# Optimization experiments

Hardware: AMD Instinct MI355X
Metric: run time of the kernel (lower is better)

The kernel has to match this reference:

```python
import jax, jax.numpy as jnp
import numpy as np

D_MODEL = 192
DEPTH = 16
D_INNER = 384   # expand=2
D_STATE = 16
D_CONV = 4
DT_RANK = 12    # ceil(192/16)
J = 42
T = 8
NUM_CLASSES = 1000
B = 64
EPS = 1e-5


def setup_inputs() -> dict:
    key = jax.random.key(0)
    ks = jax.random.split(key, 16)

    def n(k, shape, scale=0.02):
        return jax.random.normal(k, shape, jnp.float32) * scale

    dt_bias_init = float(np.log(np.expm1(0.01)))  # softplus^-1(0.01), mamba dt init
    A_init = jnp.log(jnp.tile(jnp.arange(1, D_STATE + 1, dtype=jnp.float32), (DEPTH, D_INNER, 1)))
    return {
        "x": jax.random.normal(ks[0], (B, T, J, 3), jnp.float32),
        "joint_embed_w": n(ks[1], (D_MODEL, 3)),
        "joint_embed_b": jnp.zeros((D_MODEL,), jnp.float32),
        "cls_token": n(ks[2], (1, 1, D_MODEL)),
        "spatial_pos": n(ks[3], (1, J + 1, D_MODEL)),
        "temporal_pos": n(ks[4], (1, T, D_MODEL)),
        "norm_w": jnp.ones((DEPTH, D_MODEL), jnp.float32),
        "in_proj_w": n(ks[5], (DEPTH, 2 * D_INNER, D_MODEL)),
        "conv_w": n(ks[6], (DEPTH, D_INNER, D_CONV), 0.1),
        "conv_b": jnp.zeros((DEPTH, D_INNER), jnp.float32),
        "x_proj_w": n(ks[7], (DEPTH, DT_RANK + 2 * D_STATE, D_INNER)),
        "dt_proj_w": n(ks[8], (DEPTH, D_INNER, DT_RANK), DT_RANK ** -0.5),
        "dt_proj_b": jnp.full((DEPTH, D_INNER), dt_bias_init, jnp.float32),
        "A_log": A_init,
        "Dp": jnp.ones((DEPTH, D_INNER), jnp.float32),
        "out_proj_w": n(ks[9], (DEPTH, D_MODEL, D_INNER)),
        "norm_f_w": jnp.ones((D_MODEL,), jnp.float32),
        "head_w": n(ks[10], (NUM_CLASSES, D_MODEL)),
        "head_b": jnp.zeros((NUM_CLASSES,), jnp.float32),
    }


def rmsnorm(x, w):
    return x * jax.lax.rsqrt(jnp.mean(x * x, axis=-1, keepdims=True) + EPS) * w


def mamba(x, in_w, cw, cb, xp_w, dtw, dtb, A_log, Dp, ow):
    # x: (B, L, d_model)
    Bsz, L, _ = x.shape
    xz = jnp.einsum('bld,ed->ble', x, in_w)          # (B,L,2*di)
    u, z = jnp.split(xz, 2, axis=-1)
    # depthwise causal conv over time
    uc = jnp.transpose(u, (0, 2, 1))                  # (B,di,L)
    uc = jnp.pad(uc, ((0, 0), (0, 0), (D_CONV - 1, 0)))
    uc = jax.lax.conv_general_dilated(
        uc, cw[:, None, :], (1,), 'VALID',
        dimension_numbers=('NCH', 'OIH', 'NCH'),
        feature_group_count=D_INNER) + cb[None, :, None]
    u = jax.nn.silu(jnp.transpose(uc, (0, 2, 1)))     # (B,L,di)
    dbl = jnp.einsum('bld,ed->ble', u, xp_w)          # (B,L,dt_rank+2*ds)
    dt, Bm, Cm = jnp.split(dbl, [DT_RANK, DT_RANK + D_STATE], axis=-1)
    delta = jax.nn.softplus(jnp.einsum('blr,dr->bld', dt, dtw) + dtb)  # (B,L,di)
    A = -jnp.exp(A_log)                               # (di,ds)

    def step(h, xs):
        d_t, B_t, C_t, u_t = xs                       # (B,di),(B,ds),(B,ds),(B,di)
        h = h * jnp.exp(d_t[..., None] * A) + (d_t * u_t)[..., None] * B_t[:, None, :]
        return h, jnp.einsum('bds,bs->bd', h, C_t)

    xs = (jnp.swapaxes(delta, 0, 1), jnp.swapaxes(Bm, 0, 1),
          jnp.swapaxes(Cm, 0, 1), jnp.swapaxes(u, 0, 1))
    h0 = jnp.zeros((Bsz, D_INNER, D_STATE), x.dtype)
    _, ys = jax.lax.scan(step, h0, xs)                # (L,B,di)
    y = jnp.swapaxes(ys, 0, 1) + u * Dp
    y = y * jax.nn.silu(z)
    return jnp.einsum('ble,de->bld', y, ow)


def reference(x, joint_embed_w, joint_embed_b, cls_token, spatial_pos, temporal_pos,
              norm_w, in_proj_w, conv_w, conv_b, x_proj_w, dt_proj_w, dt_proj_b,
              A_log, Dp, out_proj_w, norm_f_w, head_w, head_b):
    Bq, Tq, Jq, _ = x.shape
    xe = jnp.einsum('btjc,dc->btjd', x, joint_embed_w) + joint_embed_b
    xe = xe.reshape(Bq * Tq, Jq, D_MODEL)
    cls = jnp.broadcast_to(cls_token, (Bq * Tq, 1, D_MODEL))
    xcat = jnp.concatenate([cls, xe], axis=1) + spatial_pos   # (B*T, J+1, M)
    cls_tokens = xcat[:Bq, :1, :]
    body = xcat[:, 1:, :].reshape(Bq, Tq, Jq, D_MODEL)
    body = body.transpose(0, 2, 1, 3).reshape(Bq * Jq, Tq, D_MODEL) + temporal_pos
    body = body.reshape(Bq, Jq, Tq, D_MODEL).transpose(0, 2, 1, 3).reshape(Bq, Tq * Jq, D_MODEL)
    h = jnp.concatenate([cls_tokens, body], axis=1)           # (B, 1+T*J, M)

    residual = None
    for i in range(DEPTH):
        residual = h + residual if residual is not None else h
        hn = rmsnorm(residual, norm_w[i])
        h = mamba(hn, in_proj_w[i], conv_w[i], conv_b[i], x_proj_w[i],
                  dt_proj_w[i], dt_proj_b[i], A_log[i], Dp[i], out_proj_w[i])
    residual = h + residual
    feat = rmsnorm(residual, norm_f_w)[:, 0, :]
    return feat @ head_w.T + head_b
```

## Files before the change

kernel.cpp:

```cpp
#include <hip/hip_runtime.h>
#include <hip/hip_bf16.h>
#include <math.h>

#define B_ 64
#define T_ 8
#define J_ 42
#define L_ 337
#define D_ 192
#define E_ 384
#define S_ 16
#define R_ 12
#define DEPTH_ 16
#define NC_ 1000
#define M_ (B_*L_)
#define XZW_ (2*E_)
#define DBLW_ (R_+2*S_)
#define EPS_ 1e-5f
#define CH_ 16
#define NCH_ 22
#define EG_ (E_/8)
#define LOG2E_ 1.44269504088896f

typedef float    f32x4  __attribute__((ext_vector_type(4)));
typedef unsigned u32x4  __attribute__((ext_vector_type(4)));
typedef __bf16   bf16x8 __attribute__((ext_vector_type(8)));
typedef unsigned short ushort8 __attribute__((ext_vector_type(8)));

__device__ __forceinline__ float sigmoid_(float x){ return 1.f/(1.f+__expf(-x)); }
__device__ __forceinline__ float softplus_(float x){
  return (x > 20.f) ? x : __logf(1.f + __expf(x));
}
__device__ __forceinline__ unsigned short f2bf(float f){
  unsigned u = __float_as_uint(f);
  unsigned r = (u + 0x7fffu + ((u>>16)&1u)) >> 16;
  return (unsigned short)r;
}
__device__ __forceinline__ float bf2f(unsigned short h){
  return __uint_as_float(((unsigned)h)<<16);
}

__global__ void cvt_bf16_kernel(const float* __restrict__ in,
                                unsigned short* __restrict__ out, int n){
  int i = blockIdx.x*blockDim.x + threadIdx.x;
  if (i < n) out[i] = f2bf(in[i]);
}

__global__ void scan_prep_kernel(const float* __restrict__ dtw,
                                 const float* __restrict__ A_log,
                                 float* __restrict__ dtwT,
                                 float* __restrict__ a1v){
  int idx = blockIdx.x*blockDim.x + threadIdx.x;
  if (idx >= DEPTH_*E_) return;
  int d = idx % E_;
  int i = idx / E_;
  a1v[idx] = -__expf(A_log[((size_t)i*E_ + d)*S_]) * LOG2E_;
  #pragma unroll
  for (int r=0;r<R_;r++)
    dtwT[((size_t)i*R_ + r)*E_ + d] = dtw[((size_t)i*E_ + d)*R_ + r];
}

__global__ void embed_kernel(const float* __restrict__ x,
                             const float* __restrict__ jw,
                             const float* __restrict__ jb,
                             const float* __restrict__ cls,
                             const float* __restrict__ sp,
                             const float* __restrict__ tp,
                             float* __restrict__ res) {
  int idx = blockIdx.x*blockDim.x + threadIdx.x;
  if (idx >= M_*D_) return;
  int d = idx % D_;
  int m = idx / D_;
  int l = m % L_;
  int b = m / L_;
  float v;
  if (l == 0) {
    v = cls[d] + sp[d];
  } else {
    int lm = l-1, t = lm / J_, j = lm % J_;
    const float* xp = x + ((size_t)((b*T_+t)*J_ + j))*3;
    v = jb[d] + sp[(1+j)*D_+d] + tp[t*D_+d]
      + xp[0]*jw[d*3+0] + xp[1]*jw[d*3+1] + xp[2]*jw[d*3+2];
  }
  res[idx] = v;
}

__global__ __launch_bounds__(64) void norm0_kernel(const float* __restrict__ residual,
    const float* __restrict__ w, unsigned short* __restrict__ hn) {
  int m = blockIdx.x;
  int lane = threadIdx.x;
  size_t base = (size_t)m*D_;
  float r[3];
  float ss = 0.f;
  #pragma unroll
  for (int i=0;i<3;i++){
    int d = lane + i*64;
    r[i] = residual[base+d];
    ss += r[i]*r[i];
  }
  #pragma unroll
  for (int off=32; off>=1; off>>=1) ss += __shfl_xor(ss, off, 64);
  float sc = rsqrtf(ss*(1.f/(float)D_) + EPS_);
  #pragma unroll
  for (int i=0;i<3;i++){
    int d = lane + i*64;
    hn[base+d] = f2bf(r[i]*sc*w[d]);
  }
}

__global__ __launch_bounds__(256) void gemm_in(
    const unsigned short* __restrict__ A,
    const unsigned short* __restrict__ W,
    unsigned short* __restrict__ C)
{
  const int wave = threadIdx.x >> 6;
  const int lane = threadIdx.x & 63;
  const int row0 = blockIdx.x * 64;
  const int col0 = (blockIdx.y * 4 + wave) * 64;
  const int lr = lane & 15;
  const int lk = (lane >> 4) * 8;
  f32x4 acc[4][4] = {};
  for (int k0 = 0; k0 < D_; k0 += 32) {
    bf16x8 af[4], bfr[4];
    #pragma unroll
    for (int i=0;i<4;i++)
      af[i] = __builtin_bit_cast(bf16x8,
          *(const u32x4*)(A + (size_t)(row0 + i*16 + lr)*D_ + k0 + lk));
    #pragma unroll
    for (int j=0;j<4;j++)
      bfr[j] = __builtin_bit_cast(bf16x8,
          *(const u32x4*)(W + (size_t)(col0 + j*16 + lr)*D_ + k0 + lk));
    #pragma unroll
    for (int i=0;i<4;i++)
      #pragma unroll
      for (int j=0;j<4;j++)
        acc[i][j] = __builtin_amdgcn_mfma_f32_16x16x32_bf16(af[i], bfr[j], acc[i][j], 0, 0, 0);
  }
  const int ro = (lane >> 4) * 4;
  #pragma unroll
  for (int i=0;i<4;i++)
    #pragma unroll
    for (int j=0;j<4;j++){
      int col = col0 + j*16 + lr;
      #pragma unroll
      for (int r=0;r<4;r++){
        int row = row0 + i*16 + ro + r;
        C[(size_t)row*XZW_ + col] = f2bf(acc[i][j][r]);
      }
    }
}

__global__ __launch_bounds__(256) void gemm_xp(
    const unsigned short* __restrict__ A,
    const unsigned short* __restrict__ W,
    float* __restrict__ C)
{
  const int wave = threadIdx.x >> 6;
  const int lane = threadIdx.x & 63;
  const int row0 = blockIdx.x * 64 + wave * 16;
  const int lr = lane & 15;
  const int lk = (lane >> 4) * 8;
  const bf16x8 bzero = __builtin_bit_cast(bf16x8, (u32x4)(0u));
  f32x4 acc[3] = {};
  for (int k0 = 0; k0 < E_; k0 += 32) {
    bf16x8 af = __builtin_bit_cast(bf16x8,
        *(const u32x4*)(A + (size_t)(row0 + lr)*E_ + k0 + lk));
    #pragma unroll
    for (int j=0;j<3;j++){
      int col = j*16 + lr;
      bf16x8 bfr = (col < DBLW_) ? __builtin_bit_cast(bf16x8,
          *(const u32x4*)(W + (size_t)col*E_ + k0 + lk)) : bzero;
      acc[j] = __builtin_amdgcn_mfma_f32_16x16x32_bf16(af, bfr, acc[j], 0, 0, 0);
    }
  }
  const int ro = (lane >> 4) * 4;
  #pragma unroll
  for (int j=0;j<3;j++){
    int col = j*16 + lr;
    if (col >= DBLW_) continue;
    #pragma unroll
    for (int r=0;r<4;r++){
      int row = row0 + ro + r;
      C[(size_t)row*DBLW_ + col] = acc[j][r];
    }
  }
}

__global__ __launch_bounds__(256) void conv_silu_kernel(
    const unsigned short* __restrict__ xz,
    const float* __restrict__ cw,
    const float* __restrict__ cb,
    unsigned short* __restrict__ u2) {
  int idx = blockIdx.x*blockDim.x + threadIdx.x;
  if (idx >= M_*EG_) return;
  const int g = idx % EG_;
  const int m = idx / EG_;
  const int l = m % L_;
  const int d0 = g*8;
  float4 wr[8];
  #pragma unroll
  for (int j=0;j<8;j++) wr[j] = *(const float4*)(cw + (size_t)(d0+j)*4);
  float acc[8];
  {
    float4 b0 = *(const float4*)(cb + d0);
    float4 b1 = *(const float4*)(cb + d0 + 4);
    acc[0]=b0.x; acc[1]=b0.y; acc[2]=b0.z; acc[3]=b0.w;
    acc[4]=b1.x; acc[5]=b1.y; acc[6]=b1.z; acc[7]=b1.w;
  }
  #pragma unroll
  for (int k=0;k<4;k++){
    const int lk = l + k - 3;
    if (lk < 0) continue;
    const ushort8 v = *(const ushort8*)(xz + (size_t)(m + k - 3)*XZW_ + d0);
    const float tap0 = (k==0)?wr[0].x:(k==1)?wr[0].y:(k==2)?wr[0].z:wr[0].w;
    #pragma unroll
    for (int j=0;j<8;j++){
      float tap = (k==0)?wr[j].x:(k==1)?wr[j].y:(k==2)?wr[j].z:wr[j].w;
      acc[j] = fmaf(tap, bf2f(v[j]), acc[j]);
    }
    (void)tap0;
  }
  ushort8 o;
  #pragma unroll
  for (int j=0;j<8;j++){
    float a = acc[j];
    o[j] = f2bf(a * sigmoid_(a));
  }
  *(ushort8*)(u2 + (size_t)m*E_ + d0) = o;
}

__global__ __launch_bounds__(128) void scan_partA(
    const float* __restrict__ dbl,
    const unsigned short* __restrict__ u2,
    const float* __restrict__ dtwT,
    const float* __restrict__ dtb,
    const float* __restrict__ a1v,
    unsigned short* __restrict__ part_h,
    float* __restrict__ part_sd)
{
  const int b = blockIdx.x;
  const int d = blockIdx.y*128 + threadIdx.x;
  const int c = blockIdx.z;
  float dtw_r[R_];
  #pragma unroll
  for (int r=0;r<R_;r++) dtw_r[r] = dtwT[r*E_+d];
  const float dtb_r = dtb[d];
  const float a1 = a1v[d];
  float h[S_];
  #pragma unroll
  for (int s=0;s<S_;s++) h[s] = 0.f;
  float sum_dl = 0.f;
  const size_t m0 = (size_t)b*L_ + (size_t)c*CH_;

  for (int t=0; t<CH_; ++t) {
    const float4* dr = (const float4*)(dbl + (m0+t)*DBLW_);
    float4 q0=dr[0],q1=dr[1],q2=dr[2],q3=dr[3],q4=dr[4],q5=dr[5],q6=dr[6];
    const float u_ = bf2f(u2[(m0+t)*E_ + d]);
    float s0 = fmaf(q0.y,dtw_r[1], q0.x*dtw_r[0]);
    s0 = fmaf(q0.z,dtw_r[2], s0); s0 = fmaf(q0.w,dtw_r[3], s0);
    float s1 = fmaf(q1.y,dtw_r[5], q1.x*dtw_r[4]);
    s1 = fmaf(q1.z,dtw_r[6], s1); s1 = fmaf(q1.w,dtw_r[7], s1);
    float s2 = fmaf(q2.y,dtw_r[9], fmaf(q2.x,dtw_r[8], dtb_r));
    s2 = fmaf(q2.z,dtw_r[10], s2); s2 = fmaf(q2.w,dtw_r[11], s2);
    float dtv = softplus_((s0+s1)+s2);
    sum_dl += dtv;
    const float du = dtv * u_;
    const float rr = exp2f(dtv * a1);
    const float rr2 = rr*rr, rr3 = rr2*rr, rr4 = rr2*rr2;
    float p0=rr, p1=rr2, p2=rr3, p3=rr4;
    h[0]=fmaf(h[0],p0,du*q3.x); h[1]=fmaf(h[1],p1,du*q3.y);
    h[2]=fmaf(h[2],p2,du*q3.z); h[3]=fmaf(h[3],p3,du*q3.w);
    p0*=rr4; p1*=rr4; p2*=rr4; p3*=rr4;
    h[4]=fmaf(h[4],p0,du*q4.x); h[5]=fmaf(h[5],p1,du*q4.y);
    h[6]=fmaf(h[6],p2,du*q4.z); h[7]=fmaf(h[7],p3,du*q4.w);
    p0*=rr4; p1*=rr4; p2*=rr4; p3*=rr4;
    h[8]=fmaf(h[8],p0,du*q5.x);  h[9]=fmaf(h[9],p1,du*q5.y);
    h[10]=fmaf(h[10],p2,du*q5.z); h[11]=fmaf(h[11],p3,du*q5.w);
    p0*=rr4; p1*=rr4; p2*=rr4; p3*=rr4;
    h[12]=fmaf(h[12],p0,du*q6.x); h[13]=fmaf(h[13],p1,du*q6.y);
    h[14]=fmaf(h[14],p2,du*q6.z); h[15]=fmaf(h[15],p3,du*q6.w);
  }
  const size_t pb = (size_t)b*NCH_ + c;
  #pragma unroll
  for (int s=0;s<S_;s++) part_h[(pb*S_ + s)*E_ + d] = f2bf(h[s]);
  part_sd[pb*E_ + d] = sum_dl;
}

__global__ __launch_bounds__(256) void scan_combine(
    unsigned short* __restrict__ part_h,
    const float* __restrict__ part_sd,
    const float* __restrict__ a1v)
{
  int idx = blockIdx.x*blockDim.x + threadIdx.x;
  const int d = idx % E_;
  const int s = (idx / E_) % S_;
  const int b = idx / (E_*S_);
  const float a1s = a1v[d] * (float)(s+1);
  float hprev = 0.f;
  for (int c=0; c<NCH_-1; ++c) {
    const size_t off = (((size_t)b*NCH_ + c)*S_ + s)*E_ + d;
    const float tmp = bf2f(part_h[off]);
    part_h[off] = f2bf(hprev);
    const float sd = part_sd[((size_t)b*NCH_ + c)*E_ + d];
    hprev = fmaf(hprev, exp2f(a1s*sd), tmp);
  }
  part_h[(((size_t)b*NCH_ + NCH_-1)*S_ + s)*E_ + d] = f2bf(hprev);
}

__global__ __launch_bounds__(128) void scan_partC(
    const float* __restrict__ dbl,
    const unsigned short* __restrict__ u2,
    const unsigned short* __restrict__ xz,
    const float* __restrict__ dtwT, const float* __restrict__ dtb,
    const float* __restrict__ a1v, const float* __restrict__ Dp,
    const unsigned short* __restrict__ part_h,
    unsigned short* __restrict__ y)
{
  const int b = blockIdx.x;
  const int d = blockIdx.y*128 + threadIdx.x;
  const int c = blockIdx.z;
  const int t0 = c*CH_;
  const int nt = (t0 + CH_ <= L_) ? CH_ : (L_ - t0);
  float dtw_r[R_];
  #pragma unroll
  for (int r=0;r<R_;r++) dtw_r[r] = dtwT[r*E_+d];
  const float dtb_r = dtb[d];
  const float dpv   = Dp[d];
  const float a1 = a1v[d];
  float h[S_];
  {
    const size_t pb = (size_t)b*NCH_ + c;
    #pragma unroll
    for (int s=0;s<S_;s++) h[s] = bf2f(part_h[(pb*S_ + s)*E_ + d]);
  }
  const size_t m0 = (size_t)b*L_ + t0;

  for (int t=0; t<nt; ++t) {
    const float4* dr = (const float4*)(dbl + (m0+t)*DBLW_);
    float4 q0=dr[0],q1=dr[1],q2=dr[2],q3=dr[3],q4=dr[4],q5=dr[5],
           q6=dr[6],q7=dr[7],q8=dr[8],q9=dr[9],q10=dr[10];
    const float u_ = bf2f(u2[(m0+t)*E_ + d]);
    const float z_ = bf2f(xz[(m0+t)*XZW_ + E_ + d]);
    float s0 = fmaf(q0.y,dtw_r[1], q0.x*dtw_r[0]);
    s0 = fmaf(q0.z,dtw_r[2], s0); s0 = fmaf(q0.w,dtw_r[3], s0);
    float s1 = fmaf(q1.y,dtw_r[5], q1.x*dtw_r[4]);
    s1 = fmaf(q1.z,dtw_r[6], s1); s1 = fmaf(q1.w,dtw_r[7], s1);
    float s2 = fmaf(q2.y,dtw_r[9], fmaf(q2.x,dtw_r[8], dtb_r));
    s2 = fmaf(q2.z,dtw_r[10], s2); s2 = fmaf(q2.w,dtw_r[11], s2);
    float dtv = softplus_((s0+s1)+s2);
    const float du = dtv * u_;
    const float rr = exp2f(dtv * a1);
    const float rr2 = rr*rr, rr3 = rr2*rr, rr4 = rr2*rr2;
    float p0=rr, p1=rr2, p2=rr3, p3=rr4;
    float a0,a1_,a2,a3;
    h[0]=fmaf(h[0],p0,du*q3.x); a0=h[0]*q7.x;
    h[1]=fmaf(h[1],p1,du*q3.y); a1_=h[1]*q7.y;
    h[2]=fmaf(h[2],p2,du*q3.z); a2=h[2]*q7.z;
    h[3]=fmaf(h[3],p3,du*q3.w); a3=h[3]*q7.w;
    p0*=rr4; p1*=rr4; p2*=rr4; p3*=rr4;
    h[4]=fmaf(h[4],p0,du*q4.x); a0=fmaf(h[4],q8.x,a0);
    h[5]=fmaf(h[5],p1,du*q4.y); a1_=fmaf(h[5],q8.y,a1_);
    h[6]=fmaf(h[6],p2,du*q4.z); a2=fmaf(h[6],q8.z,a2);
    h[7]=fmaf(h[7],p3,du*q4.w); a3=fmaf(h[7],q8.w,a3);
    p0*=rr4; p1*=rr4; p2*=rr4; p3*=rr4;
    h[8]=fmaf(h[8],p0,du*q5.x);  a0=fmaf(h[8],q9.x,a0);
    h[9]=fmaf(h[9],p1,du*q5.y);  a1_=fmaf(h[9],q9.y,a1_);
    h[10]=fmaf(h[10],p2,du*q5.z); a2=fmaf(h[10],q9.z,a2);
    h[11]=fmaf(h[11],p3,du*q5.w); a3=fmaf(h[11],q9.w,a3);
    p0*=rr4; p1*=rr4; p2*=rr4; p3*=rr4;
    h[12]=fmaf(h[12],p0,du*q6.x); a0=fmaf(h[12],q10.x,a0);
    h[13]=fmaf(h[13],p1,du*q6.y); a1_=fmaf(h[13],q10.y,a1_);
    h[14]=fmaf(h[14],p2,du*q6.z); a2=fmaf(h[14],q10.z,a2);
    h[15]=fmaf(h[15],p3,du*q6.w); a3=fmaf(h[15],q10.w,a3);
    const float accv = (a0+a1_)+(a2+a3);
    const float yv = fmaf(u_, dpv, accv) * (z_ * sigmoid_(z_));
    y[(m0+t)*E_ + d] = f2bf(yv);
  }
}

__global__ __launch_bounds__(192) void gemm_out_fused(
    const unsigned short* __restrict__ A,
    const unsigned short* __restrict__ W,
    float* __restrict__ residual,
    const float* __restrict__ wnext,
    unsigned short* __restrict__ hn)
{
  const int wave = threadIdx.x >> 6;
  const int lane = threadIdx.x & 63;
  const int row0 = blockIdx.x * 64;
  const int col0 = wave * 64;
  const int lr = lane & 15;
  const int lk = (lane >> 4) * 8;
  f32x4 acc[4][4] = {};
  for (int k0 = 0; k0 < E_; k0 += 32) {
    bf16x8 af[4], bfr[4];
    #pragma unroll
    for (int i=0;i<4;i++)
      af[i] = __builtin_bit_cast(bf16x8,
          *(const u32x4*)(A + (size_t)(row0 + i*16 + lr)*E_ + k0 + lk));
    #pragma unroll
    for (int j=0;j<4;j++)
      bfr[j] = __builtin_bit_cast(bf16x8,
          *(const u32x4*)(W + (size_t)(col0 + j*16 + lr)*E_ + k0 + lk));
    #pragma unroll
    for (int i=0;i<4;i++)
      #pragma unroll
      for (int j=0;j<4;j++)
        acc[i][j] = __builtin_amdgcn_mfma_f32_16x16x32_bf16(af[i], bfr[j], acc[i][j], 0, 0, 0);
  }
  const int ro = (lane >> 4) * 4;
  __shared__ float rs[3][64];
  float wn[4];
  #pragma unroll
  for (int j=0;j<4;j++) wn[j] = wnext[col0 + j*16 + lr];
  #pragma unroll
  for (int i=0;i<4;i++){
    #pragma unroll
    for (int r=0;r<4;r++){
      int row = row0 + i*16 + ro + r;
      float psum = 0.f;
      #pragma unroll
      for (int j=0;j<4;j++){
        int col = col0 + j*16 + lr;
        float v = residual[(size_t)row*D_ + col] + acc[i][j][r];
        acc[i][j][r] = v;
        residual[(size_t)row*D_ + col] = v;
        psum = fmaf(v, v, psum);
      }
      psum += __shfl_xor(psum, 1);
      psum += __shfl_xor(psum, 2);
      psum += __shfl_xor(psum, 4);
      psum += __shfl_xor(psum, 8);
      if (lr == 0) rs[wave][i*16 + ro + r] = psum;
    }
  }
  __syncthreads();
  #pragma unroll
  for (int i=0;i<4;i++){
    #pragma unroll
    for (int r=0;r<4;r++){
      int rloc = i*16 + ro + r;
      float tot = rs[0][rloc] + rs[1][rloc] + rs[2][rloc];
      float sc = rsqrtf(tot*(1.f/(float)D_) + EPS_);
      int row = row0 + rloc;
      #pragma unroll
      for (int j=0;j<4;j++){
        int col = col0 + j*16 + lr;
        hn[(size_t)row*D_ + col] = f2bf(acc[i][j][r]*sc*wn[j]);
      }
    }
  }
}

__global__ __launch_bounds__(64) void final_norm_kernel(const float* __restrict__ residual,
    const float* __restrict__ w, float* __restrict__ feat) {
  int b = blockIdx.x;
  int lane = threadIdx.x;
  size_t base = (size_t)b*L_*D_;
  float r[3]; float ss = 0.f;
  #pragma unroll
  for (int i=0;i<3;i++){
    int d = lane + i*64;
    r[i] = residual[base+d];
    ss += r[i]*r[i];
  }
  #pragma unroll
  for (int off=32; off>=1; off>>=1) ss += __shfl_xor(ss, off, 64);
  float sc = rsqrtf(ss*(1.f/(float)D_) + EPS_);
  #pragma unroll
  for (int i=0;i<3;i++){
    int d = lane + i*64;
    feat[b*D_ + d] = r[i]*sc*w[d];
  }
}

__global__ __launch_bounds__(256) void head_kernel(const float* __restrict__ feat,
    const float* __restrict__ hw, const float* __restrict__ hb,
    float* __restrict__ out) {
  __shared__ float fs[D_];
  int b = blockIdx.x;
  for (int i=threadIdx.x;i<D_;i+=blockDim.x) fs[i] = feat[b*D_+i];
  __syncthreads();
  for (int n=threadIdx.x;n<NC_;n+=blockDim.x){
    float acc = hb[n];
    #pragma unroll 4
    for (int k=0;k<D_;k++) acc += fs[k]*hw[(size_t)n*D_+k];
    out[(size_t)b*NC_+n] = acc;
  }
}

extern "C" void kernel_launch(void* const* d_in, const int* in_sizes, int n_in,
                              void* d_out, int out_size, void* d_ws, size_t ws_size,
                              hipStream_t stream) {
  const float* x        = (const float*)d_in[0];
  const float* jw       = (const float*)d_in[1];
  const float* jb       = (const float*)d_in[2];
  const float* cls      = (const float*)d_in[3];
  const float* sp       = (const float*)d_in[4];
  const float* tp       = (const float*)d_in[5];
  const float* norm_w   = (const float*)d_in[6];
  const float* in_w     = (const float*)d_in[7];
  const float* conv_w   = (const float*)d_in[8];
  const float* conv_b   = (const float*)d_in[9];
  const float* xp_w     = (const float*)d_in[10];
  const float* dt_w     = (const float*)d_in[11];
  const float* dt_b     = (const float*)d_in[12];
  const float* A_log    = (const float*)d_in[13];
  const float* Dp       = (const float*)d_in[14];
  const float* out_w    = (const float*)d_in[15];
  const float* norm_f_w = (const float*)d_in[16];
  const float* head_w   = (const float*)d_in[17];
  const float* head_b   = (const float*)d_in[18];
  float* out = (float*)d_out;

  float* ws = (float*)d_ws;
  float* residual = ws;
  float* dbl      = residual + (size_t)M_*D_;
  float* feat     = dbl      + (size_t)M_*DBLW_;
  float* part_sd  = feat     + (size_t)B_*D_;
  float* dtwT     = part_sd  + (size_t)B_*NCH_*E_;
  float* a1v      = dtwT     + (size_t)DEPTH_*R_*E_;
  unsigned short* bw = (unsigned short*)(a1v + (size_t)DEPTH_*E_);
  unsigned short* hn     = bw;
  unsigned short* xz     = hn     + (size_t)M_*D_;
  unsigned short* u2     = xz     + (size_t)M_*XZW_;
  unsigned short* ybuf   = u2     + (size_t)M_*E_;
  unsigned short* part_h = ybuf   + (size_t)M_*E_;
  unsigned short* w_in   = part_h + (size_t)B_*NCH_*S_*E_;
  unsigned short* w_xp   = w_in   + (size_t)DEPTH_*XZW_*D_;
  unsigned short* w_out  = w_xp   + (size_t)DEPTH_*DBLW_*E_;

  {
    int n1 = DEPTH_*XZW_*D_;
    int n2 = DEPTH_*DBLW_*E_;
    int n3 = DEPTH_*D_*E_;
    cvt_bf16_kernel<<<(n1+255)/256, 256, 0, stream>>>(in_w,  w_in,  n1);
    cvt_bf16_kernel<<<(n2+255)/256, 256, 0, stream>>>(xp_w,  w_xp,  n2);
    cvt_bf16_kernel<<<(n3+255)/256, 256, 0, stream>>>(out_w, w_out, n3);
    scan_prep_kernel<<<(DEPTH_*E_+255)/256, 256, 0, stream>>>(dt_w, A_log, dtwT, a1v);
  }

  embed_kernel<<<(M_*D_+255)/256, 256, 0, stream>>>(x, jw, jb, cls, sp, tp, residual);
  norm0_kernel<<<M_, 64, 0, stream>>>(residual, norm_w, hn);

  for (int i = 0; i < DEPTH_; ++i) {
    gemm_in<<<dim3(M_/64, XZW_/256), 256, 0, stream>>>(
        hn, w_in + (size_t)i*XZW_*D_, xz);
    conv_silu_kernel<<<(M_*EG_+255)/256, 256, 0, stream>>>(
        xz, conv_w + (size_t)i*E_*4, conv_b + (size_t)i*E_, u2);
    gemm_xp<<<M_/64, 256, 0, stream>>>(
        u2, w_xp + (size_t)i*DBLW_*E_, dbl);
    scan_partA<<<dim3(B_, E_/128, NCH_-1), 128, 0, stream>>>(
        dbl, u2, dtwT + (size_t)i*R_*E_, dt_b + (size_t)i*E_,
        a1v + (size_t)i*E_, part_h, part_sd);
    scan_combine<<<(B_*S_*E_)/256, 256, 0, stream>>>(
        part_h, part_sd, a1v + (size_t)i*E_);
    scan_partC<<<dim3(B_, E_/128, NCH_), 128, 0, stream>>>(
        dbl, u2, xz, dtwT + (size_t)i*R_*E_, dt_b + (size_t)i*E_,
        a1v + (size_t)i*E_, Dp + (size_t)i*E_, part_h, ybuf);
    const float* wnext = (i+1 < DEPTH_) ? (norm_w + (size_t)(i+1)*D_) : norm_f_w;
    gemm_out_fused<<<M_/64, 192, 0, stream>>>(
        ybuf, w_out + (size_t)i*D_*E_, residual, wnext, hn);
  }

  final_norm_kernel<<<B_, 64, 0, stream>>>(residual, norm_f_w, feat);
  head_kernel<<<B_, 256, 0, stream>>>(feat, head_w, head_b, out);
}
```

Before: 2.727 ms.

## Fuse conv+SiLU into x_proj GEMM via LDS tile, merge final norm into head

```diff
diff --git a/kernel.cpp b/kernel.cpp
--- a/kernel.cpp
+++ b/kernel.cpp
@@ -19,6 +19,7 @@
 #define CH_ 16
 #define NCH_ 22
 #define EG_ (E_/8)
+#define USTR_ (E_+8)
 #define LOG2E_ 1.44269504088896f
 
 typedef float    f32x4  __attribute__((ext_vector_type(4)));
@@ -149,27 +150,71 @@
     }
 }
 
-__global__ __launch_bounds__(256) void gemm_xp(
-    const unsigned short* __restrict__ A,
+__global__ __launch_bounds__(256) void conv_xp_kernel(
+    const unsigned short* __restrict__ xz,
+    const float* __restrict__ cw,
+    const float* __restrict__ cb,
     const unsigned short* __restrict__ W,
-    float* __restrict__ C)
+    unsigned short* __restrict__ u2,
+    float* __restrict__ dbl)
 {
-  const int wave = threadIdx.x >> 6;
-  const int lane = threadIdx.x & 63;
-  const int row0 = blockIdx.x * 64 + wave * 16;
+  __shared__ unsigned short us[64*USTR_];
+  const int row0 = blockIdx.x*64;
+  const int tid = threadIdx.x;
+  #pragma unroll
+  for (int it=0; it<12; ++it) {
+    const int task = tid + it*256;
+    const int r = task / EG_;
+    const int g = task % EG_;
+    const int m = row0 + r;
+    const int l = m % L_;
+    const int d0 = g*8;
+    float acc[8];
+    {
+      float4 b0 = *(const float4*)(cb + d0);
+      float4 b1 = *(const float4*)(cb + d0 + 4);
+      acc[0]=b0.x; acc[1]=b0.y; acc[2]=b0.z; acc[3]=b0.w;
+      acc[4]=b1.x; acc[5]=b1.y; acc[6]=b1.z; acc[7]=b1.w;
+    }
+    float4 wr[8];
+    #pragma unroll
+    for (int j=0;j<8;j++) wr[j] = *(const float4*)(cw + (size_t)(d0+j)*4);
+    #pragma unroll
+    for (int k=0;k<4;k++){
+      const int lk_ = l + k - 3;
+      if (lk_ < 0) continue;
+      const ushort8 v = *(const ushort8*)(xz + (size_t)(m + k - 3)*XZW_ + d0);
+      #pragma unroll
+      for (int j=0;j<8;j++){
+        float tap = (k==0)?wr[j].x:(k==1)?wr[j].y:(k==2)?wr[j].z:wr[j].w;
+        acc[j] = fmaf(tap, bf2f(v[j]), acc[j]);
+      }
+    }
+    ushort8 o;
+    #pragma unroll
+    for (int j=0;j<8;j++){
+      float a = acc[j];
+      o[j] = f2bf(a * sigmoid_(a));
+    }
+    *(ushort8*)(&us[r*USTR_ + d0]) = o;
+    *(ushort8*)(u2 + (size_t)m*E_ + d0) = o;
+  }
+  __syncthreads();
+  const int wave = tid >> 6;
+  const int lane = tid & 63;
   const int lr = lane & 15;
   const int lk = (lane >> 4) * 8;
   const bf16x8 bzero = __builtin_bit_cast(bf16x8, (u32x4)(0u));
-  f32x4 acc[3] = {};
+  f32x4 acc3[3] = {};
   for (int k0 = 0; k0 < E_; k0 += 32) {
     bf16x8 af = __builtin_bit_cast(bf16x8,
-        *(const u32x4*)(A + (size_t)(row0 + lr)*E_ + k0 + lk));
+        *(const u32x4*)(&us[(wave*16 + lr)*USTR_ + k0 + lk]));
     #pragma unroll
     for (int j=0;j<3;j++){
       int col = j*16 + lr;
       bf16x8 bfr = (col < DBLW_) ? __builtin_bit_cast(bf16x8,
           *(const u32x4*)(W + (size_t)col*E_ + k0 + lk)) : bzero;
-      acc[j] = __builtin_amdgcn_mfma_f32_16x16x32_bf16(af, bfr, acc[j], 0, 0, 0);
+      acc3[j] = __builtin_amdgcn_mfma_f32_16x16x32_bf16(af, bfr, acc3[j], 0, 0, 0);
     }
   }
   const int ro = (lane >> 4) * 4;
@@ -178,54 +223,11 @@
     int col = j*16 + lr;
     if (col >= DBLW_) continue;
     #pragma unroll
-    for (int r=0;r<4;r++){
-      int row = row0 + ro + r;
-      C[(size_t)row*DBLW_ + col] = acc[j][r];
-    }
-  }
-}
-
-__global__ __launch_bounds__(256) void conv_silu_kernel(
-    const unsigned short* __restrict__ xz,
-    const float* __restrict__ cw,
-    const float* __restrict__ cb,
-    unsigned short* __restrict__ u2) {
-  int idx = blockIdx.x*blockDim.x + threadIdx.x;
-  if (idx >= M_*EG_) return;
-  const int g = idx % EG_;
-  const int m = idx / EG_;
-  const int l = m % L_;
-  const int d0 = g*8;
-  float4 wr[8];
-  #pragma unroll
-  for (int j=0;j<8;j++) wr[j] = *(const float4*)(cw + (size_t)(d0+j)*4);
-  float acc[8];
-  {
-    float4 b0 = *(const float4*)(cb + d0);
-    float4 b1 = *(const float4*)(cb + d0 + 4);
-    acc[0]=b0.x; acc[1]=b0.y; acc[2]=b0.z; acc[3]=b0.w;
-    acc[4]=b1.x; acc[5]=b1.y; acc[6]=b1.z; acc[7]=b1.w;
-  }
-  #pragma unroll
-  for (int k=0;k<4;k++){
-    const int lk = l + k - 3;
-    if (lk < 0) continue;
-    const ushort8 v = *(const ushort8*)(xz + (size_t)(m + k - 3)*XZW_ + d0);
-    const float tap0 = (k==0)?wr[0].x:(k==1)?wr[0].y:(k==2)?wr[0].z:wr[0].w;
-    #pragma unroll
-    for (int j=0;j<8;j++){
-      float tap = (k==0)?wr[j].x:(k==1)?wr[j].y:(k==2)?wr[j].z:wr[j].w;
-      acc[j] = fmaf(tap, bf2f(v[j]), acc[j]);
-    }
-    (void)tap0;
-  }
-  ushort8 o;
-  #pragma unroll
-  for (int j=0;j<8;j++){
-    float a = acc[j];
-    o[j] = f2bf(a * sigmoid_(a));
-  }
-  *(ushort8*)(u2 + (size_t)m*E_ + d0) = o;
+    for (int r2=0;r2<4;r2++){
+      int row = row0 + wave*16 + ro + r2;
+      dbl[(size_t)row*DBLW_ + col] = acc3[j][r2];
+    }
+  }
 }
 
 __global__ __launch_bounds__(128) void scan_partA(
@@ -451,36 +453,26 @@
   }
 }
 
-__global__ __launch_bounds__(64) void final_norm_kernel(const float* __restrict__ residual,
-    const float* __restrict__ w, float* __restrict__ feat) {
-  int b = blockIdx.x;
-  int lane = threadIdx.x;
-  size_t base = (size_t)b*L_*D_;
-  float r[3]; float ss = 0.f;
-  #pragma unroll
-  for (int i=0;i<3;i++){
-    int d = lane + i*64;
-    r[i] = residual[base+d];
-    ss += r[i]*r[i];
-  }
-  #pragma unroll
-  for (int off=32; off>=1; off>>=1) ss += __shfl_xor(ss, off, 64);
-  float sc = rsqrtf(ss*(1.f/(float)D_) + EPS_);
-  #pragma unroll
-  for (int i=0;i<3;i++){
-    int d = lane + i*64;
-    feat[b*D_ + d] = r[i]*sc*w[d];
-  }
-}
-
-__global__ __launch_bounds__(256) void head_kernel(const float* __restrict__ feat,
+__global__ __launch_bounds__(256) void final_head_kernel(
+    const float* __restrict__ residual, const float* __restrict__ w,
     const float* __restrict__ hw, const float* __restrict__ hb,
     float* __restrict__ out) {
   __shared__ float fs[D_];
-  int b = blockIdx.x;
-  for (int i=threadIdx.x;i<D_;i+=blockDim.x) fs[i] = feat[b*D_+i];
+  __shared__ float red[4];
+  const int b = blockIdx.x;
+  const int tid = threadIdx.x;
+  const size_t base = (size_t)b*L_*D_;
+  float v = (tid < D_) ? residual[base+tid] : 0.f;
+  float ss = v*v;
+  #pragma unroll
+  for (int off=32; off>=1; off>>=1) ss += __shfl_xor(ss, off, 64);
+  if ((tid & 63) == 0) red[tid>>6] = ss;
   __syncthreads();
-  for (int n=threadIdx.x;n<NC_;n+=blockDim.x){
+  const float tot = red[0]+red[1]+red[2]+red[3];
+  const float sc = rsqrtf(tot*(1.f/(float)D_) + EPS_);
+  if (tid < D_) fs[tid] = v*sc*w[tid];
+  __syncthreads();
+  for (int n=tid;n<NC_;n+=256){
     float acc = hb[n];
     #pragma unroll 4
     for (int k=0;k<D_;k++) acc += fs[k]*hw[(size_t)n*D_+k];
@@ -515,8 +507,7 @@
   float* ws = (float*)d_ws;
   float* residual = ws;
   float* dbl      = residual + (size_t)M_*D_;
-  float* feat     = dbl      + (size_t)M_*DBLW_;
-  float* part_sd  = feat     + (size_t)B_*D_;
+  float* part_sd  = dbl      + (size_t)M_*DBLW_;
   float* dtwT     = part_sd  + (size_t)B_*NCH_*E_;
   float* a1v      = dtwT     + (size_t)DEPTH_*R_*E_;
   unsigned short* bw = (unsigned short*)(a1v + (size_t)DEPTH_*E_);
@@ -545,10 +536,9 @@
   for (int i = 0; i < DEPTH_; ++i) {
     gemm_in<<<dim3(M_/64, XZW_/256), 256, 0, stream>>>(
         hn, w_in + (size_t)i*XZW_*D_, xz);
-    conv_silu_kernel<<<(M_*EG_+255)/256, 256, 0, stream>>>(
-        xz, conv_w + (size_t)i*E_*4, conv_b + (size_t)i*E_, u2);
-    gemm_xp<<<M_/64, 256, 0, stream>>>(
-        u2, w_xp + (size_t)i*DBLW_*E_, dbl);
+    conv_xp_kernel<<<M_/64, 256, 0, stream>>>(
+        xz, conv_w + (size_t)i*E_*4, conv_b + (size_t)i*E_,
+        w_xp + (size_t)i*DBLW_*E_, u2, dbl);
     scan_partA<<<dim3(B_, E_/128, NCH_-1), 128, 0, stream>>>(
         dbl, u2, dtwT + (size_t)i*R_*E_, dt_b + (size_t)i*E_,
         a1v + (size_t)i*E_, part_h, part_sd);
@@ -562,6 +552,5 @@
         ybuf, w_out + (size_t)i*D_*E_, residual, wnext, hn);
   }
 
-  final_norm_kernel<<<B_, 64, 0, stream>>>(residual, norm_f_w, feat);
-  head_kernel<<<B_, 256, 0, stream>>>(feat, head_w, head_b, out);
-}
+  final_head_kernel<<<B_, 256, 0, stream>>>(residual, norm_f_w, head_w, head_b, out);
+}
```

Result: slower. 2.968 ms (+8.9%).
